# Performance work log

Measured on AMD Instinct MI355X. Metric: run time of the kernel, lower is better.

The kernel has to match this reference:

```python
import jax, jax.numpy as jnp
import numpy as np

QMAX = 127.0

def setup_inputs() -> dict:
    key = jax.random.key(0)
    kx, kw, ks = jax.random.split(key, 3)
    B, S, D_IN, D_OUT = 4, 2048, 4096, 4096
    x = jax.random.normal(kx, (B, S, D_IN), dtype=jnp.float16)
    # int8 weight buffer, same distribution as torch.randint(-127, 127)
    weight = jax.random.randint(kw, (D_OUT, D_IN), -127, 127, dtype=jnp.int32).astype(jnp.int8)
    # per-output-channel weight scales (fp16 buffer); small positive values
    weight_scales = (jax.random.uniform(ks, (D_OUT,), dtype=jnp.float32) * 0.01 + 1e-4).astype(jnp.float16)
    return {"x": x, "weight": weight, "weight_scales": weight_scales}

def reference(x, weight, weight_scales):
    # x: [B, S, D_in] fp16; weight: [D_out, D_in] int8; weight_scales: [D_out] fp16
    x32 = x.astype(jnp.float32)
    # dynamic per-token absmax quantization: scale = absmax / 127
    absmax = jnp.max(jnp.abs(x32), axis=-1, keepdims=True)      # [B, S, 1]
    x_scales = jnp.maximum(absmax / QMAX, 1e-8)
    q = jnp.round(x32 / x_scales)                                # in [-127, 127]
    q = jnp.clip(q, -QMAX, QMAX).astype(jnp.int8)
    # int8 GEMM accumulated in int32 (cupy.matmul on int32 in the original)
    y = jnp.einsum('bsk,nk->bsn', q.astype(jnp.int32), weight.astype(jnp.int32),
                   preferred_element_type=jnp.int32)             # [B, S, D_out]
    # dequant: per-token activation scale * per-channel weight scale
    y = y.astype(jnp.float32) * x_scales * weight_scales.astype(jnp.float32)[None, None, :]
    return y.astype(jnp.float16)
```

## Files before the change

kernel.cpp:

```cpp
#include <hip/hip_runtime.h>
#include <stdint.h>

typedef int int32x4 __attribute__((ext_vector_type(4)));

constexpr int K_DIM = 4096;
constexpr int N_DIM = 4096;
constexpr float QMAXF = 127.0f;

__global__ __launch_bounds__(256) void quant_rows(const float* __restrict__ x,
                                                  int8_t* __restrict__ q,
                                                  float* __restrict__ scales) {
    const int row = blockIdx.x;
    const int tid = threadIdx.x;
    const size_t base = (size_t)row * K_DIM;

    const float4* xv = reinterpret_cast<const float4*>(x + base);
    float4 v[4];
#pragma unroll
    for (int i = 0; i < 4; ++i) v[i] = xv[tid + 256 * i];

    float m = 0.0f;
#pragma unroll
    for (int i = 0; i < 4; ++i)
        m = fmaxf(m, fmaxf(fmaxf(fabsf(v[i].x), fabsf(v[i].y)),
                           fmaxf(fabsf(v[i].z), fabsf(v[i].w))));
#pragma unroll
    for (int off = 32; off > 0; off >>= 1) m = fmaxf(m, __shfl_xor(m, off));

    __shared__ float wmax[4];
    if ((tid & 63) == 0) wmax[tid >> 6] = m;
    __syncthreads();
    const float am = fmaxf(fmaxf(wmax[0], wmax[1]), fmaxf(wmax[2], wmax[3]));
    const float scale = fmaxf(am * (1.0f / 127.0f), 1e-8f);
    if (tid == 0) scales[row] = scale;
    const float inv = 1.0f / scale;

    int* qw = reinterpret_cast<int*>(q + base);
#pragma unroll
    for (int i = 0; i < 4; ++i) {
        float f0 = fminf(QMAXF, fmaxf(-QMAXF, rintf(v[i].x * inv)));
        float f1 = fminf(QMAXF, fmaxf(-QMAXF, rintf(v[i].y * inv)));
        float f2 = fminf(QMAXF, fmaxf(-QMAXF, rintf(v[i].z * inv)));
        float f3 = fminf(QMAXF, fmaxf(-QMAXF, rintf(v[i].w * inv)));
        int b0 = ((int)f0) & 255, b1 = ((int)f1) & 255;
        int b2 = ((int)f2) & 255, b3 = ((int)f3) & 255;
        qw[tid + 256 * i] = b0 | (b1 << 8) | (b2 << 16) | (b3 << 24);
    }
}

__global__ __launch_bounds__(256) void pack_w(const int* __restrict__ w,
                                              int8_t* __restrict__ w8) {
    const int idx = blockIdx.x * 256 + threadIdx.x;
    const int4 v = reinterpret_cast<const int4*>(w)[idx];
    int packed = (v.x & 255) | ((v.y & 255) << 8) | ((v.z & 255) << 16) | ((v.w & 255) << 24);
    reinterpret_cast<int*>(w8)[idx] = packed;
}

constexpr int BM = 256, BN = 256, BKB = 128;
constexpr int NT = K_DIM / BKB;

#define GLL(src, dst)                                                          \
    __builtin_amdgcn_global_load_lds(                                          \
        (const __attribute__((address_space(1))) unsigned int*)(src),          \
        (__attribute__((address_space(3))) unsigned int*)(dst), 16, 0, 0)

#define MFMA_I8(a, b, c) __builtin_amdgcn_mfma_i32_16x16x64_i8((a), (b), (c), 0, 0, 0)

__global__ __launch_bounds__(512, 2) void w8a8_gemm256(
        const int8_t* __restrict__ A, const int8_t* __restrict__ B,
        const float* __restrict__ asc, const float* __restrict__ wsc,
        float* __restrict__ C, int M) {
    extern __shared__ int8_t lds[];

    const int tid  = threadIdx.x;
    const int lane = tid & 63;
    const int wave = tid >> 6;

    const int nwg = gridDim.x;
    const int bid = blockIdx.x;
    const int swz = (bid & 7) * (nwg >> 3) + (bid >> 3);
    const int NB  = N_DIM / BN;
    const int brow = (swz / NB) * BM;
    const int bcol = (swz % NB) * BN;

    const int wm = wave >> 2;
    const int wn = wave & 3;
    const int l15 = lane & 15;
    const int ls  = lane >> 4;

    const int rowin = tid >> 3;
    const int gsl   = ((tid & 7) ^ (rowin & 7)) * 16;
    const int8_t* gA = A + (size_t)(brow + rowin) * K_DIM + gsl;
    const int8_t* gB = B + (size_t)(bcol + rowin) * K_DIM + gsl;
    const size_t chunk_g = (size_t)64 * K_DIM;
    const int segb = wave * 1024;

    const int sbase = ((ls ^ (l15 & 7)) * 16);
    const int offA0 = (wm * 128 + l15) * BKB + sbase;
    const int offB0 = (wn * 64  + l15) * BKB + sbase;

    int32x4 acc[8][4];
#pragma unroll
    for (int i = 0; i < 8; ++i)
#pragma unroll
        for (int j = 0; j < 4; ++j) acc[i][j] = (int32x4){0, 0, 0, 0};

#pragma unroll
    for (int c = 0; c < 4; ++c) {
        GLL(gA + c * chunk_g, lds + c * 8192 + segb);
        GLL(gB + c * chunk_g, lds + 65536 + c * 8192 + segb);
    }
    asm volatile("s_waitcnt vmcnt(0)" ::: "memory");
    __builtin_amdgcn_s_barrier();

    int32x4 af[8], bf01[4], bf23[4];

    for (int t = 0; t < NT; ++t) {
        const int8_t* Ab = lds + (t & 1) * 32768;
        const int8_t* Bb = lds + 65536 + (t & 1) * 32768;
        const int  p1   = (t + 1) & 1;
        const bool pf   = (t + 1 < NT);
        const size_t kk = (size_t)(t + 1) * BKB;
        int8_t* dA = lds + p1 * 32768;
        int8_t* dB = lds + 65536 + p1 * 32768;

        if (pf) {
            GLL(gA + kk,               dA + segb);
            GLL(gA + kk + 2 * chunk_g, dA + 16384 + segb);
            GLL(gB + kk,               dB + segb);
        }
#pragma unroll
        for (int mi = 0; mi < 4; ++mi) {
            af[2 * mi]     = *(const int32x4*)(Ab + ((offA0 + mi * 2048)));
            af[2 * mi + 1] = *(const int32x4*)(Ab + ((offA0 + mi * 2048) ^ 64));
        }
#pragma unroll
        for (int ni = 0; ni < 2; ++ni) {
            bf01[2 * ni]     = *(const int32x4*)(Bb + ((offB0 + ni * 2048)));
            bf01[2 * ni + 1] = *(const int32x4*)(Bb + ((offB0 + ni * 2048) ^ 64));
        }
        __builtin_amdgcn_s_barrier();
        asm volatile("s_waitcnt lgkmcnt(0)" ::: "memory");
        __builtin_amdgcn_s_setprio(1);
#pragma unroll
        for (int mi = 0; mi < 4; ++mi)
#pragma unroll
            for (int ni = 0; ni < 2; ++ni)
#pragma unroll
                for (int kh = 0; kh < 2; ++kh)
                    acc[mi][ni] = MFMA_I8(af[2 * mi + kh], bf01[2 * ni + kh], acc[mi][ni]);
        __builtin_amdgcn_s_setprio(0);
        if (t < NT - 1) asm volatile("s_waitcnt vmcnt(3)" ::: "memory");
        else            asm volatile("s_waitcnt vmcnt(0)" ::: "memory");
        __builtin_amdgcn_s_barrier();

        if (pf) {
            GLL(gB + kk + 1 * chunk_g, dB + 8192 + segb);
            GLL(gB + kk + 2 * chunk_g, dB + 16384 + segb);
            GLL(gB + kk + 3 * chunk_g, dB + 24576 + segb);
        }
#pragma unroll
        for (int ni = 0; ni < 2; ++ni) {
            bf23[2 * ni]     = *(const int32x4*)(Bb + ((offB0 + (ni + 2) * 2048)));
            bf23[2 * ni + 1] = *(const int32x4*)(Bb + ((offB0 + (ni + 2) * 2048) ^ 64));
        }
        __builtin_amdgcn_s_barrier();
        asm volatile("s_waitcnt lgkmcnt(0)" ::: "memory");
        __builtin_amdgcn_s_setprio(1);
#pragma unroll
        for (int mi = 0; mi < 4; ++mi)
#pragma unroll
            for (int ni = 0; ni < 2; ++ni)
#pragma unroll
                for (int kh = 0; kh < 2; ++kh)
                    acc[mi][ni + 2] = MFMA_I8(af[2 * mi + kh], bf23[2 * ni + kh], acc[mi][ni + 2]);
        __builtin_amdgcn_s_setprio(0);
        __builtin_amdgcn_s_barrier();

        if (pf) {
            GLL(gA + kk + 1 * chunk_g, dA + 8192 + segb);
            GLL(gA + kk + 3 * chunk_g, dA + 24576 + segb);
        }
#pragma unroll
        for (int mi = 0; mi < 4; ++mi) {
            af[2 * mi]     = *(const int32x4*)(Ab + ((offA0 + (mi + 4) * 2048)));
            af[2 * mi + 1] = *(const int32x4*)(Ab + ((offA0 + (mi + 4) * 2048) ^ 64));
        }
        __builtin_amdgcn_s_barrier();
        asm volatile("s_waitcnt lgkmcnt(0)" ::: "memory");
        __builtin_amdgcn_s_setprio(1);
#pragma unroll
        for (int mi = 0; mi < 4; ++mi)
#pragma unroll
            for (int ni = 0; ni < 2; ++ni)
#pragma unroll
                for (int kh = 0; kh < 2; ++kh)
                    acc[mi + 4][ni + 2] = MFMA_I8(af[2 * mi + kh], bf23[2 * ni + kh], acc[mi + 4][ni + 2]);
        __builtin_amdgcn_s_setprio(0);
        __builtin_amdgcn_s_barrier();

        __builtin_amdgcn_s_setprio(1);
#pragma unroll
        for (int mi = 0; mi < 4; ++mi)
#pragma unroll
            for (int ni = 0; ni < 2; ++ni)
#pragma unroll
                for (int kh = 0; kh < 2; ++kh)
                    acc[mi + 4][ni] = MFMA_I8(af[2 * mi + kh], bf01[2 * ni + kh], acc[mi + 4][ni]);
        __builtin_amdgcn_s_setprio(0);
        asm volatile("s_waitcnt vmcnt(2)" ::: "memory");
        __builtin_amdgcn_s_barrier();
    }

    const int c0  = lane & 15;
    const int rr0 = (lane >> 4) * 4;
#pragma unroll
    for (int ni = 0; ni < 4; ++ni) {
        const int col = bcol + wn * 64 + ni * 16 + c0;
        const float ws = wsc[col];
#pragma unroll
        for (int mi = 0; mi < 8; ++mi) {
            const int rowb = brow + wm * 128 + mi * 16 + rr0;
#pragma unroll
            for (int r = 0; r < 4; ++r) {
                const int row = rowb + r;
                float o = (float)acc[mi][ni][r] * asc[row] * ws;
                o = (float)(_Float16)o;
                C[(size_t)row * N_DIM + col] = o;
            }
        }
    }
}

extern "C" void kernel_launch(void* const* d_in, const int* in_sizes, int n_in,
                              void* d_out, int out_size, void* d_ws, size_t ws_size,
                              hipStream_t stream) {
    const float* x   = (const float*)d_in[0];
    const int*   w   = (const int*)d_in[1];
    const float* wsc = (const float*)d_in[2];
    float* out = (float*)d_out;

    const int K = K_DIM;
    const int M = in_sizes[0] / K;
    const int N = N_DIM;

    int8_t* q   = (int8_t*)d_ws;
    int8_t* w8  = (int8_t*)d_ws + (size_t)M * K;
    float*  asc = (float*)((char*)d_ws + (size_t)M * K + (size_t)N * K);

    quant_rows<<<M, 256, 0, stream>>>(x, q, asc);
    pack_w<<<(N * (K / 4)) / 256, 256, 0, stream>>>(w, w8);
    const int grid = (M / BM) * (N / BN);
    w8a8_gemm256<<<grid, 512, 131072, stream>>>(q, w8, asc, wsc, out, M);
}
```

Before: 186.2 us.

## Restructure GEMM main loop with rotating A-fragment registers and fewer barriers

Replaces the four-phase main loop, which had about six barriers per K-step and staggered global-to-LDS prefetches, with a single pass that uses two barriers per step. All B fragments are loaded once per step, and A fragments stream through a three-slot register ring. Graded lgkmcnt waits let LDS reads overlap the MFMAs. The next tile's A is prefetched at the start of each step and its B midway, with vmcnt waits tuned to match. This aims to cut barrier stalls and expose more LDS and MFMA overlap, at the cost of a different register-pressure profile and tighter wait-count bookkeeping.

```diff
diff --git a/kernel.cpp b/kernel.cpp
--- a/kernel.cpp
+++ b/kernel.cpp
@@ -106,110 +106,68 @@
         for (int j = 0; j < 4; ++j) acc[i][j] = (int32x4){0, 0, 0, 0};
 
 #pragma unroll
-    for (int c = 0; c < 4; ++c) {
-        GLL(gA + c * chunk_g, lds + c * 8192 + segb);
-        GLL(gB + c * chunk_g, lds + 65536 + c * 8192 + segb);
-    }
-    asm volatile("s_waitcnt vmcnt(0)" ::: "memory");
-    __builtin_amdgcn_s_barrier();
-
-    int32x4 af[8], bf01[4], bf23[4];
+    for (int c = 0; c < 4; ++c) GLL(gA + c * chunk_g, lds + c * 8192 + segb);
+#pragma unroll
+    for (int c = 0; c < 4; ++c) GLL(gB + c * chunk_g, lds + 65536 + c * 8192 + segb);
+
+    int32x4 bf[4][2];
+    int32x4 afr[3][2];
 
     for (int t = 0; t < NT; ++t) {
         const int8_t* Ab = lds + (t & 1) * 32768;
         const int8_t* Bb = lds + 65536 + (t & 1) * 32768;
-        const int  p1   = (t + 1) & 1;
-        const bool pf   = (t + 1 < NT);
+        int8_t* dA = lds + ((t + 1) & 1) * 32768;
+        int8_t* dB = lds + 65536 + ((t + 1) & 1) * 32768;
+        const bool pf = (t + 1 < NT);
         const size_t kk = (size_t)(t + 1) * BKB;
-        int8_t* dA = lds + p1 * 32768;
-        int8_t* dB = lds + 65536 + p1 * 32768;
-
+
+        __builtin_amdgcn_s_barrier();
         if (pf) {
-            GLL(gA + kk,               dA + segb);
-            GLL(gA + kk + 2 * chunk_g, dA + 16384 + segb);
-            GLL(gB + kk,               dB + segb);
-        }
-#pragma unroll
-        for (int mi = 0; mi < 4; ++mi) {
-            af[2 * mi]     = *(const int32x4*)(Ab + ((offA0 + mi * 2048)));
-            af[2 * mi + 1] = *(const int32x4*)(Ab + ((offA0 + mi * 2048) ^ 64));
-        }
-#pragma unroll
-        for (int ni = 0; ni < 2; ++ni) {
-            bf01[2 * ni]     = *(const int32x4*)(Bb + ((offB0 + ni * 2048)));
-            bf01[2 * ni + 1] = *(const int32x4*)(Bb + ((offB0 + ni * 2048) ^ 64));
+#pragma unroll
+            for (int c = 0; c < 4; ++c) GLL(gA + kk + c * chunk_g, dA + c * 8192 + segb);
+            asm volatile("s_waitcnt vmcnt(4)" ::: "memory");
+        } else {
+            asm volatile("s_waitcnt vmcnt(0)" ::: "memory");
         }
         __builtin_amdgcn_s_barrier();
-        asm volatile("s_waitcnt lgkmcnt(0)" ::: "memory");
-        __builtin_amdgcn_s_setprio(1);
-#pragma unroll
-        for (int mi = 0; mi < 4; ++mi)
-#pragma unroll
-            for (int ni = 0; ni < 2; ++ni)
-#pragma unroll
-                for (int kh = 0; kh < 2; ++kh)
-                    acc[mi][ni] = MFMA_I8(af[2 * mi + kh], bf01[2 * ni + kh], acc[mi][ni]);
-        __builtin_amdgcn_s_setprio(0);
-        if (t < NT - 1) asm volatile("s_waitcnt vmcnt(3)" ::: "memory");
-        else            asm volatile("s_waitcnt vmcnt(0)" ::: "memory");
-        __builtin_amdgcn_s_barrier();
-
-        if (pf) {
-            GLL(gB + kk + 1 * chunk_g, dB + 8192 + segb);
-            GLL(gB + kk + 2 * chunk_g, dB + 16384 + segb);
-            GLL(gB + kk + 3 * chunk_g, dB + 24576 + segb);
-        }
-#pragma unroll
-        for (int ni = 0; ni < 2; ++ni) {
-            bf23[2 * ni]     = *(const int32x4*)(Bb + ((offB0 + (ni + 2) * 2048)));
-            bf23[2 * ni + 1] = *(const int32x4*)(Bb + ((offB0 + (ni + 2) * 2048) ^ 64));
-        }
-        __builtin_amdgcn_s_barrier();
-        asm volatile("s_waitcnt lgkmcnt(0)" ::: "memory");
-        __builtin_amdgcn_s_setprio(1);
-#pragma unroll
-        for (int mi = 0; mi < 4; ++mi)
-#pragma unroll
-            for (int ni = 0; ni < 2; ++ni)
-#pragma unroll
-                for (int kh = 0; kh < 2; ++kh)
-                    acc[mi][ni + 2] = MFMA_I8(af[2 * mi + kh], bf23[2 * ni + kh], acc[mi][ni + 2]);
-        __builtin_amdgcn_s_setprio(0);
-        __builtin_amdgcn_s_barrier();
-
-        if (pf) {
-            GLL(gA + kk + 1 * chunk_g, dA + 8192 + segb);
-            GLL(gA + kk + 3 * chunk_g, dA + 24576 + segb);
-        }
-#pragma unroll
-        for (int mi = 0; mi < 4; ++mi) {
-            af[2 * mi]     = *(const int32x4*)(Ab + ((offA0 + (mi + 4) * 2048)));
-            af[2 * mi + 1] = *(const int32x4*)(Ab + ((offA0 + (mi + 4) * 2048) ^ 64));
-        }
-        __builtin_amdgcn_s_barrier();
-        asm volatile("s_waitcnt lgkmcnt(0)" ::: "memory");
-        __builtin_amdgcn_s_setprio(1);
-#pragma unroll
-        for (int mi = 0; mi < 4; ++mi)
-#pragma unroll
-            for (int ni = 0; ni < 2; ++ni)
-#pragma unroll
-                for (int kh = 0; kh < 2; ++kh)
-                    acc[mi + 4][ni + 2] = MFMA_I8(af[2 * mi + kh], bf23[2 * ni + kh], acc[mi + 4][ni + 2]);
-        __builtin_amdgcn_s_setprio(0);
-        __builtin_amdgcn_s_barrier();
-
-        __builtin_amdgcn_s_setprio(1);
-#pragma unroll
-        for (int mi = 0; mi < 4; ++mi)
-#pragma unroll
-            for (int ni = 0; ni < 2; ++ni)
-#pragma unroll
-                for (int kh = 0; kh < 2; ++kh)
-                    acc[mi + 4][ni] = MFMA_I8(af[2 * mi + kh], bf01[2 * ni + kh], acc[mi + 4][ni]);
-        __builtin_amdgcn_s_setprio(0);
-        asm volatile("s_waitcnt vmcnt(2)" ::: "memory");
-        __builtin_amdgcn_s_barrier();
+
+#pragma unroll
+        for (int ni = 0; ni < 4; ++ni) {
+            bf[ni][0] = *(const int32x4*)(Bb + ((offB0 + ni * 2048)));
+            bf[ni][1] = *(const int32x4*)(Bb + ((offB0 + ni * 2048) ^ 64));
+        }
+#pragma unroll
+        for (int mi = 0; mi < 2; ++mi) {
+            afr[mi][0] = *(const int32x4*)(Ab + ((offA0 + mi * 2048)));
+            afr[mi][1] = *(const int32x4*)(Ab + ((offA0 + mi * 2048) ^ 64));
+        }
+
+#pragma unroll
+        for (int mi = 0; mi < 8; ++mi) {
+            if (mi < 6) {
+                const int s = (mi + 2) % 3;
+                afr[s][0] = *(const int32x4*)(Ab + ((offA0 + (mi + 2) * 2048)));
+                afr[s][1] = *(const int32x4*)(Ab + ((offA0 + (mi + 2) * 2048) ^ 64));
+            }
+            if (mi == 4 && pf) {
+#pragma unroll
+                for (int c = 0; c < 4; ++c)
+                    GLL(gB + kk + c * chunk_g, dB + c * 8192 + segb);
+            }
+            if (mi < 6)      asm volatile("s_waitcnt lgkmcnt(4)" ::: "memory");
+            else if (mi == 6) asm volatile("s_waitcnt lgkmcnt(2)" ::: "memory");
+            else              asm volatile("s_waitcnt lgkmcnt(0)" ::: "memory");
+            __builtin_amdgcn_sched_barrier(0);
+
+            const int cs = mi % 3;
+            __builtin_amdgcn_s_setprio(1);
+#pragma unroll
+            for (int ni = 0; ni < 4; ++ni) {
+                acc[mi][ni] = MFMA_I8(afr[cs][0], bf[ni][0], acc[mi][ni]);
+                acc[mi][ni] = MFMA_I8(afr[cs][1], bf[ni][1], acc[mi][ni]);
+            }
+            __builtin_amdgcn_s_setprio(0);
+        }
     }
 
     const int c0  = lane & 15;
```

Result: no change. 182.5 us (-2.0%).
